# Optimization experiments

Hardware: AMD Instinct MI355X
Metric: run time of the kernel (lower is better)

Reference implementation:

```python
import jax, jax.numpy as jnp
import numpy as np
from jax import lax

V, E, H, K = 100000, 256, 512, 12
B, T = 64, 256
START, END, PAD = 10, 11, 0
NEG = -100000.0


def setup_inputs() -> dict:
    key = jax.random.key(0)
    ks = jax.random.split(key, 16)
    Hd = H // 2
    def n(k, shape, s=0.1):
        return jax.random.normal(k, shape, jnp.float32) * s
    sentence = jax.random.randint(ks[0], (B, T), 0, V)
    sentence_chars = jnp.zeros((B, T, 16), jnp.int32)
    emb = jax.random.normal(ks[1], (V, E), jnp.float32)
    Wih_f, Whh_f = n(ks[2], (4 * Hd, E)), n(ks[3], (4 * Hd, Hd))
    bih_f, bhh_f = n(ks[4], (4 * Hd,)), n(ks[5], (4 * Hd,))
    Wih_b, Whh_b = n(ks[6], (4 * Hd, E)), n(ks[7], (4 * Hd, Hd))
    bih_b, bhh_b = n(ks[8], (4 * Hd,)), n(ks[9], (4 * Hd,))
    Wp, bp = n(ks[10], (K, H)), n(ks[11], (K,))
    # transitions[i, j] = score of transitioning from tag j to tag i
    trans = jax.random.normal(ks[12], (K, K), jnp.float32)
    trans = trans.at[START, :].set(NEG)
    trans = trans.at[:, END].set(NEG)
    trans = trans.at[:, PAD].set(NEG)
    trans = trans.at[PAD, :].set(NEG)
    trans = trans.at[PAD, PAD].set(0.0)
    trans = trans.at[PAD, END].set(0.0)
    h0 = jax.random.normal(ks[13], (2, B, Hd), jnp.float32)
    c0 = jax.random.normal(ks[14], (2, B, Hd), jnp.float32)
    return dict(sentence=sentence, sentence_chars=sentence_chars, emb=emb,
                Wih_f=Wih_f, Whh_f=Whh_f, bih_f=bih_f, bhh_f=bhh_f,
                Wih_b=Wih_b, Whh_b=Whh_b, bih_b=bih_b, bhh_b=bhh_b,
                Wp=Wp, bp=bp, transitions=trans, h0=h0, c0=c0)


def _lstm_dir(x, Wih, Whh, bih, bhh, h, c, reverse):
    # x: [B, T, E] -> hs: [B, T, Hd]; PyTorch LSTM gate order i,f,g,o
    def step(carry, xt):
        h, c = carry
        g = xt @ Wih.T + bih + h @ Whh.T + bhh
        i, f, gg, o = jnp.split(g, 4, axis=-1)
        c = jax.nn.sigmoid(f) * c + jax.nn.sigmoid(i) * jnp.tanh(gg)
        h = jax.nn.sigmoid(o) * jnp.tanh(c)
        return (h, c), h
    _, hs = lax.scan(step, (h, c), jnp.swapaxes(x, 0, 1), reverse=reverse)
    return jnp.swapaxes(hs, 0, 1)


def _viterbi(features, transitions, lengths):
    b, t, k = features.shape
    score0 = jnp.full((b, k), -10000.0, features.dtype).at[:, START].set(0.0)
    def step(score, feat_t):
        m = score[:, None, :] + transitions[None]  # [B, K(to), K(from)]
        bptr = jnp.argmax(m, axis=-1)              # [B, K]
        new = jnp.max(m, axis=-1) + feat_t
        return new, bptr
    final, bptrs = lax.scan(step, score0, jnp.swapaxes(features, 0, 1))  # bptrs [T,B,K]
    best_score = jnp.max(final, axis=-1)
    best_tag = jnp.argmax(final, axis=-1)
    ts = jnp.arange(t)
    def backtrack(x, inp):
        tt, bp = inp  # bp: [B, K]
        emit = x      # p_t (valid where tt < length)
        nxt = jnp.take_along_axis(bp, x[:, None], axis=1)[:, 0]
        x = jnp.where(tt < lengths, nxt, x)
        return x, emit
    _, ps = lax.scan(backtrack, best_tag, (ts, bptrs), reverse=True)  # [T, B]
    paths = jnp.swapaxes(ps, 0, 1)
    paths = jnp.where(jnp.arange(t)[None, :] < lengths[:, None], paths, -1)
    return paths, best_score


def reference(sentence, sentence_chars, emb, Wih_f, Whh_f, bih_f, bhh_f,
              Wih_b, Whh_b, bih_b, bhh_b, Wp, bp, transitions, h0, c0):
    mask = sentence > 0
    lengths = mask.sum(axis=1)
    x = emb[sentence]  # [B, T, E]
    hf = _lstm_dir(x, Wih_f, Whh_f, bih_f, bhh_f, h0[0], c0[0], False)
    hb = _lstm_dir(x, Wih_b, Whh_b, bih_b, bhh_b, h0[1], c0[1], True)
    feats = jnp.concatenate([hf, hb], axis=-1) @ Wp.T + bp  # [B, T, K]
    paths, best_score = _viterbi(feats, transitions, lengths)
    return paths, best_score
```

## Files before the change

### kernel.cpp

```cpp
#include <hip/hip_runtime.h>


#define NB 64
#define NT 256
#define NKTAG 12
#define START_TAG 10
#define KK_SLAB 32
#define KK_REG 16
#define KK_STRM 8

typedef unsigned short u16;
typedef _Float16 half2v __attribute__((ext_vector_type(2)));
typedef _Float16 half8 __attribute__((ext_vector_type(8)));
typedef float f32x4 __attribute__((ext_vector_type(4)));

__device__ __forceinline__ float b2f(u16 u) {
  union { unsigned int i; float f; } v; v.i = ((unsigned int)u) << 16; return v.f;
}
__device__ __forceinline__ u16 f2b(float f) {
  union { float f; unsigned int i; } v; v.f = f;
  unsigned int r = v.i + 0x7FFFu + ((v.i >> 16) & 1u);
  return (u16)(r >> 16);
}
__device__ __forceinline__ u16 f2h(float f) {
  union { _Float16 h; u16 u; } v; v.h = (_Float16)f; return v.u;
}
__device__ __forceinline__ unsigned int pkh(float x, float y) {
  return (unsigned int)f2h(x) | ((unsigned int)f2h(y) << 16);
}
__device__ __forceinline__ float fsig(float x) { return 1.0f / (1.0f + __expf(-x)); }
__device__ __forceinline__ float ftanh(float x) { return 2.0f / (1.0f + __expf(-2.0f * x)) - 1.0f; }

__device__ __forceinline__ float dot2h(unsigned int a, unsigned int b, float c) {
#if __has_builtin(__builtin_amdgcn_fdot2)
  union { unsigned int u; half2v h; } va, vb;
  va.u = a; vb.u = b;
  return __builtin_amdgcn_fdot2(va.h, vb.h, c, false);
#else
  float d;
  asm("v_dot2_f32_f16 %0, %1, %2, %3" : "=v"(d) : "v"(a), "v"(b), "v"(c));
  return d;
#endif
}

__global__ __launch_bounds__(256) void pack_whh(const float* __restrict__ Whf,
                                                const float* __restrict__ Whb,
                                                uint4* __restrict__ WT) {
  int gid = blockIdx.x * 256 + threadIdx.x;
  int d = gid >> 15;
  int rem = gid & 32767;
  int kk = rem >> 8, j = rem & 255;
  const float* W = d ? Whb : Whf;
  int k0 = kk * 2;
  uint4 o;
  o.x = pkh(W[(size_t)j * 256 + k0],         W[(size_t)j * 256 + k0 + 1]);
  o.y = pkh(W[(size_t)(j + 256) * 256 + k0], W[(size_t)(j + 256) * 256 + k0 + 1]);
  o.z = pkh(W[(size_t)(j + 512) * 256 + k0], W[(size_t)(j + 512) * 256 + k0 + 1]);
  o.w = pkh(W[(size_t)(j + 768) * 256 + k0], W[(size_t)(j + 768) * 256 + k0 + 1]);
  WT[gid] = o;
}

__global__ __launch_bounds__(256) void gemm_x(const int* __restrict__ sent,
                                              const float* __restrict__ emb,
                                              const float* __restrict__ Wf,
                                              const float* __restrict__ Wb,
                                              const float* __restrict__ bihf,
                                              const float* __restrict__ bhhf,
                                              const float* __restrict__ bihb,
                                              const float* __restrict__ bhhb,
                                              u16* __restrict__ X4) {
  __shared__ _Float16 A_lds[128][40];
  __shared__ _Float16 B_lds[64][40];
  __shared__ int tok[128];
  int tid = threadIdx.x;
  int in = blockIdx.x;
  int im = blockIdx.y;
  if (tid < 128) tok[tid] = sent[im * 128 + tid];

  int w = tid >> 6, l = tid & 63;
  int lrow = l & 15, lk = l >> 4;
  f32x4 acc[2][4];
#pragma unroll
  for (int mt = 0; mt < 2; ++mt)
#pragma unroll
    for (int nt = 0; nt < 4; ++nt) acc[mt][nt] = (f32x4)0.0f;

  int arow = tid >> 1, akh = tid & 1;
  int brow = tid & 63, bkq = tid >> 6;
  int ngb = in * 64 + brow;
  const float* wrow = (ngb < 1024) ? (Wf + (size_t)ngb * 256) : (Wb + (size_t)(ngb - 1024) * 256);

  for (int kc = 0; kc < 8; ++kc) {
    int k0 = kc * 32;
    __syncthreads();
    {
      const float* ap = emb + (size_t)tok[arow] * 256 + k0 + akh * 16;
#pragma unroll
      for (int q = 0; q < 2; ++q) {
        float4 v0 = *(const float4*)(ap + q * 8);
        float4 v1 = *(const float4*)(ap + q * 8 + 4);
        uint4 pk;
        pk.x = pkh(v0.x, v0.y); pk.y = pkh(v0.z, v0.w);
        pk.z = pkh(v1.x, v1.y); pk.w = pkh(v1.z, v1.w);
        *(uint4*)&A_lds[arow][akh * 16 + q * 8] = pk;
      }
    }
    {
      float4 v0 = *(const float4*)(wrow + k0 + bkq * 8);
      float4 v1 = *(const float4*)(wrow + k0 + bkq * 8 + 4);
      uint4 pk;
      pk.x = pkh(v0.x, v0.y); pk.y = pkh(v0.z, v0.w);
      pk.z = pkh(v1.x, v1.y); pk.w = pkh(v1.z, v1.w);
      *(uint4*)&B_lds[brow][bkq * 8] = pk;
    }
    __syncthreads();
    half8 af[2], bf[4];
#pragma unroll
    for (int mt = 0; mt < 2; ++mt)
      af[mt] = *(const half8*)&A_lds[w * 32 + mt * 16 + lrow][lk * 8];
#pragma unroll
    for (int nt = 0; nt < 4; ++nt)
      bf[nt] = *(const half8*)&B_lds[nt * 16 + lrow][lk * 8];
#pragma unroll
    for (int mt = 0; mt < 2; ++mt)
#pragma unroll
      for (int nt = 0; nt < 4; ++nt)
        acc[mt][nt] = __builtin_amdgcn_mfma_f32_16x16x32_f16(af[mt], bf[nt], acc[mt][nt], 0, 0, 0);
  }
#pragma unroll
  for (int nt = 0; nt < 4; ++nt) {
    int n = in * 64 + nt * 16 + lrow;
    int d = n >> 10, rr = n & 1023;
    int gate = rr >> 8, j = rr & 255;
    float bias = d ? (bihb[rr] + bhhb[rr]) : (bihf[rr] + bhhf[rr]);
#pragma unroll
    for (int mt = 0; mt < 2; ++mt) {
#pragma unroll
      for (int r = 0; r < 4; ++r) {
        int i = im * 128 + w * 32 + mt * 16 + lk * 4 + r;
        int bb = i >> 8, tt = i & 255;
        size_t o = ((((size_t)d * NT + tt) * NB + bb) * 256 + j) * 4 + gate;
        X4[o] = f2b(acc[mt][nt][r] + bias);
      }
    }
  }
}

__global__ __launch_bounds__(1024, 4) void lstm_scan(const uint4* __restrict__ WT,
                                                     const ushort4* __restrict__ X4,
                                                     const float* __restrict__ h0,
                                                     const float* __restrict__ c0,
                                                     void* __restrict__ H, int h32) {
  int d = blockIdx.x >> 6, b = blockIdx.x & 63;
  int tid = threadIdx.x;
  int jj = tid & 255, g = tid >> 8;
  __shared__ uint4 wlds[KK_SLAB * 256];
  __shared__ uint4 h2s4[32];
  __shared__ float4 plds[3][256];
  const uint4* Ws = WT + (size_t)d * 32768;
  for (int e = tid; e < KK_SLAB * 256; e += 1024) wlds[e] = Ws[e];
  uint4 wreg[KK_REG];
#pragma unroll
  for (int r = 0; r < KK_REG; ++r)
    wreg[r] = Ws[(size_t)(KK_SLAB + g * KK_REG + r) * 256 + jj];
  float c = 0.f;
  if (g == 0) c = c0[((size_t)d * NB + b) * 256 + jj];
  if (tid < 256) ((u16*)h2s4)[tid] = f2h(h0[((size_t)d * NB + b) * 256 + tid]);
  __syncthreads();
  for (int s = 0; s < NT; ++s) {
    int t = d ? (NT - 1 - s) : s;
    ushort4 xg = make_ushort4(0, 0, 0, 0);
    if (g == 0) xg = X4[(((size_t)d * NT + t) * NB + b) * 256 + jj];
    float ai = 0.f, af = 0.f, ag = 0.f, ao = 0.f;
    {
      uint4 hc0 = h2s4[24 + g * 2], hc1 = h2s4[24 + g * 2 + 1];
      unsigned int hp[8] = {hc0.x, hc0.y, hc0.z, hc0.w, hc1.x, hc1.y, hc1.z, hc1.w};
      const uint4* Wp_ = Ws + (size_t)(96 + g * 8) * 256 + jj;
#pragma unroll
      for (int u = 0; u < KK_STRM; ++u) {
        uint4 wv = Wp_[(size_t)u * 256];
        ai = dot2h(wv.x, hp[u], ai); af = dot2h(wv.y, hp[u], af);
        ag = dot2h(wv.z, hp[u], ag); ao = dot2h(wv.w, hp[u], ao);
      }
    }
    {
      uint4 ha0 = h2s4[g * 2], ha1 = h2s4[g * 2 + 1];
      unsigned int hp[8] = {ha0.x, ha0.y, ha0.z, ha0.w, ha1.x, ha1.y, ha1.z, ha1.w};
#pragma unroll
      for (int r = 0; r < 8; ++r) {
        uint4 wv = wlds[((g * 8 + r) << 8) | jj];
        ai = dot2h(wv.x, hp[r], ai); af = dot2h(wv.y, hp[r], af);
        ag = dot2h(wv.z, hp[r], ag); ao = dot2h(wv.w, hp[r], ao);
      }
    }
    {
      uint4 hb0 = h2s4[8 + g * 4], hb1 = h2s4[8 + g * 4 + 1];
      uint4 hb2 = h2s4[8 + g * 4 + 2], hb3 = h2s4[8 + g * 4 + 3];
      unsigned int hp[16] = {hb0.x, hb0.y, hb0.z, hb0.w, hb1.x, hb1.y, hb1.z, hb1.w,
                             hb2.x, hb2.y, hb2.z, hb2.w, hb3.x, hb3.y, hb3.z, hb3.w};
#pragma unroll
      for (int r = 0; r < KK_REG; ++r) {
        uint4 wv = wreg[r];
        ai = dot2h(wv.x, hp[r], ai); af = dot2h(wv.y, hp[r], af);
        ag = dot2h(wv.z, hp[r], ag); ao = dot2h(wv.w, hp[r], ao);
      }
    }
    if (g) plds[g - 1][jj] = make_float4(ai, af, ag, ao);
    __syncthreads();
    if (g == 0) {
      float4 p0 = plds[0][jj], p1 = plds[1][jj], p2 = plds[2][jj];
      ai += p0.x + p1.x + p2.x + b2f(xg.x);
      af += p0.y + p1.y + p2.y + b2f(xg.y);
      ag += p0.z + p1.z + p2.z + b2f(xg.z);
      ao += p0.w + p1.w + p2.w + b2f(xg.w);
      float ii = fsig(ai), ff = fsig(af), gg = ftanh(ag), oo = fsig(ao);
      c = ff * c + ii * gg;
      float h = oo * ftanh(c);
      ((u16*)h2s4)[jj] = f2h(h);
      size_t ho = (((size_t)d * NB + b) * NT + t) * 256 + jj;
      if (h32) ((float*)H)[ho] = h; else ((u16*)H)[ho] = f2b(h);
    }
    __syncthreads();
  }
}

__global__ __launch_bounds__(384) void feats_kernel(const void* __restrict__ H, int h32,
                                                    const float* __restrict__ Wp,
                                                    const float* __restrict__ bp,
                                                    float* __restrict__ FT) {
  __shared__ float hbuf[32][516];
  int tid = threadIdx.x;
  int i0 = blockIdx.x * 32;
  for (int idx = tid; idx < 32 * 512; idx += 384) {
    int row = idx >> 9, col = idx & 511;
    int i = i0 + row;
    int b = i >> 8, t = i & 255;
    int dd = col >> 8, jj = col & 255;
    size_t ho = (((size_t)dd * NB + b) * NT + t) * 256 + jj;
    hbuf[row][col] = h32 ? ((const float*)H)[ho] : b2f(((const u16*)H)[ho]);
  }
  __syncthreads();
  int row = tid / 12, k = tid - row * 12;
  const float* wp = Wp + (size_t)k * 512;
  float s = 0.f;
  for (int ccol = 0; ccol < 512; ++ccol) s += hbuf[row][ccol] * wp[ccol];
  int i = i0 + row;
  FT[(size_t)i * NKTAG + k] = s + bp[k];
}

__global__ __launch_bounds__(64) void viterbi_kernel(const float* __restrict__ FT,
                                                     const float* __restrict__ trans,
                                                     const int* __restrict__ sent,
                                                     float* __restrict__ out) {
  int b = blockIdx.x, tid = threadIdx.x;
  __shared__ float trans_s[12][12];
  __shared__ float s_s[12];
  __shared__ unsigned char bp_s[256][12];
  __shared__ int path_s[256];
  for (int idx = tid; idx < 144; idx += 64) trans_s[idx / 12][idx % 12] = trans[idx];
  int cnt = 0;
#pragma unroll
  for (int q = 0; q < 4; ++q) cnt += (sent[b * NT + q * 64 + tid] > 0) ? 1 : 0;
  for (int off = 32; off; off >>= 1) cnt += __shfl_down(cnt, off);
  int len = __shfl(cnt, 0);
  if (tid < 12) s_s[tid] = (tid == START_TAG) ? 0.f : -10000.f;
  __syncthreads();
  for (int t = 0; t < NT; ++t) {
    float best = 0.f, f = 0.f;
    int barg = 0;
    if (tid < 12) {
      f = FT[((size_t)b * NT + t) * NKTAG + tid];
      best = s_s[0] + trans_s[tid][0];
      barg = 0;
#pragma unroll
      for (int fr = 1; fr < 12; ++fr) {
        float v = s_s[fr] + trans_s[tid][fr];
        if (v > best) { best = v; barg = fr; }
      }
    }
    __syncthreads();
    if (tid < 12) {
      s_s[tid] = best + f;
      bp_s[t][tid] = (unsigned char)barg;
    }
    __syncthreads();
  }
  if (tid == 0) {
    float bs = s_s[0];
    int bt = 0;
    for (int k = 1; k < 12; ++k)
      if (s_s[k] > bs) { bs = s_s[k]; bt = k; }
    out[NB * NT + b] = bs;
    int x = bt;
    for (int tt = NT - 1; tt >= 0; --tt) {
      path_s[tt] = x;
      int nxt = bp_s[tt][x];
      if (tt < len) x = nxt;
    }
  }
  __syncthreads();
#pragma unroll
  for (int q = 0; q < 4; ++q) {
    int t = q * 64 + tid;
    out[b * NT + t] = (t < len) ? (float)path_s[t] : -1.0f;
  }
}

extern "C" void kernel_launch(void* const* d_in, const int* in_sizes, int n_in,
                              void* d_out, int out_size, void* d_ws, size_t ws_size,
                              hipStream_t stream) {
  (void)in_sizes; (void)n_in; (void)out_size;
  const int*   sent  = (const int*)d_in[0];
  const float* emb   = (const float*)d_in[2];
  const float* Wih_f = (const float*)d_in[3];
  const float* Whh_f = (const float*)d_in[4];
  const float* bih_f = (const float*)d_in[5];
  const float* bhh_f = (const float*)d_in[6];
  const float* Wih_b = (const float*)d_in[7];
  const float* Whh_b = (const float*)d_in[8];
  const float* bih_b = (const float*)d_in[9];
  const float* bhh_b = (const float*)d_in[10];
  const float* Wp    = (const float*)d_in[11];
  const float* bp    = (const float*)d_in[12];
  const float* trans = (const float*)d_in[13];
  const float* h0    = (const float*)d_in[14];
  const float* c0    = (const float*)d_in[15];
  float* out = (float*)d_out;

  char* w = (char*)d_ws;
  u16*   X4  = (u16*)w;
  uint4* WTH = (uint4*)(w + 67108864);
  float* FT  = (float*)(w + 67108864 + 1048576);
  void*  H   = (void*)(w + 67108864 + 1048576 + 786432);
  const size_t base = 67108864 + 1048576 + 786432;
  int h32 = (ws_size >= base + (size_t)33554432) ? 1 : 0;

  pack_whh<<<dim3(256), dim3(256), 0, stream>>>(Whh_f, Whh_b, WTH);
  gemm_x<<<dim3(32, 128), dim3(256), 0, stream>>>(sent, emb, Wih_f, Wih_b,
                                                  bih_f, bhh_f, bih_b, bhh_b, X4);
  lstm_scan<<<dim3(128), dim3(1024), 0, stream>>>(WTH, (const ushort4*)X4, h0, c0, H, h32);
  feats_kernel<<<dim3(512), dim3(384), 0, stream>>>(H, h32, Wp, bp, FT);
  viterbi_kernel<<<dim3(64), dim3(64), 0, stream>>>(FT, trans, sent, out);
}
```

Measured before the change: 658.8 us.

## Coalesce gemm_x output via LDS staging and use fp16 hidden states in feats

```diff
diff --git a/kernel.cpp b/kernel.cpp
--- a/kernel.cpp
+++ b/kernel.cpp
@@ -45,7 +45,17 @@
 
 __global__ __launch_bounds__(256) void pack_whh(const float* __restrict__ Whf,
                                                 const float* __restrict__ Whb,
-                                                uint4* __restrict__ WT) {
+                                                const float* __restrict__ Wp,
+                                                uint4* __restrict__ WT,
+                                                unsigned int* __restrict__ WpH) {
+  if (blockIdx.x == 256) {
+    for (int it = 0; it < 12; ++it) {
+      int idx = it * 256 + threadIdx.x;
+      int k = idx >> 8, cc = idx & 255;
+      WpH[idx] = pkh(Wp[(size_t)k * 512 + 2 * cc], Wp[(size_t)k * 512 + 2 * cc + 1]);
+    }
+    return;
+  }
   int gid = blockIdx.x * 256 + threadIdx.x;
   int d = gid >> 15;
   int rem = gid & 32767;
@@ -72,9 +82,11 @@
   __shared__ _Float16 A_lds[128][40];
   __shared__ _Float16 B_lds[64][40];
   __shared__ int tok[128];
+  __shared__ u16 Xs[128][80];
   int tid = threadIdx.x;
   int in = blockIdx.x;
   int im = blockIdx.y;
+  int d = in >> 4, j0 = (in & 15) * 16;
   if (tid < 128) tok[tid] = sent[im * 128 + tid];
 
   int w = tid >> 6, l = tid & 63;
@@ -87,8 +99,8 @@
 
   int arow = tid >> 1, akh = tid & 1;
   int brow = tid & 63, bkq = tid >> 6;
-  int ngb = in * 64 + brow;
-  const float* wrow = (ngb < 1024) ? (Wf + (size_t)ngb * 256) : (Wb + (size_t)(ngb - 1024) * 256);
+  int r_w = ((brow >> 4) << 8) + j0 + (brow & 15);
+  const float* wrow = (d ? Wb : Wf) + (size_t)r_w * 256;
 
   for (int kc = 0; kc < 8; ++kc) {
     int k0 = kc * 32;
@@ -127,30 +139,40 @@
       for (int nt = 0; nt < 4; ++nt)
         acc[mt][nt] = __builtin_amdgcn_mfma_f32_16x16x32_f16(af[mt], bf[nt], acc[mt][nt], 0, 0, 0);
   }
+  float bias[4];
 #pragma unroll
   for (int nt = 0; nt < 4; ++nt) {
-    int n = in * 64 + nt * 16 + lrow;
-    int d = n >> 10, rr = n & 1023;
-    int gate = rr >> 8, j = rr & 255;
-    float bias = d ? (bihb[rr] + bhhb[rr]) : (bihf[rr] + bhhf[rr]);
-#pragma unroll
-    for (int mt = 0; mt < 2; ++mt) {
-#pragma unroll
-      for (int r = 0; r < 4; ++r) {
-        int i = im * 128 + w * 32 + mt * 16 + lk * 4 + r;
-        int bb = i >> 8, tt = i & 255;
-        size_t o = ((((size_t)d * NT + tt) * NB + bb) * 256 + j) * 4 + gate;
-        X4[o] = f2b(acc[mt][nt][r] + bias);
-      }
-    }
-  }
+    int rr = nt * 256 + j0 + lrow;
+    bias[nt] = d ? (bihb[rr] + bhhb[rr]) : (bihf[rr] + bhhf[rr]);
+  }
+  __syncthreads();
+#pragma unroll
+  for (int mt = 0; mt < 2; ++mt)
+#pragma unroll
+    for (int r = 0; r < 4; ++r) {
+      int row = w * 32 + mt * 16 + lk * 4 + r;
+      uint2 pk;
+      pk.x = (unsigned int)f2b(acc[mt][0][r] + bias[0]) |
+             ((unsigned int)f2b(acc[mt][1][r] + bias[1]) << 16);
+      pk.y = (unsigned int)f2b(acc[mt][2][r] + bias[2]) |
+             ((unsigned int)f2b(acc[mt][3][r] + bias[3]) << 16);
+      *(uint2*)&Xs[row][lrow * 4] = pk;
+    }
+  __syncthreads();
+  int frow = tid >> 1, fh = tid & 1;
+  int i = im * 128 + frow;
+  int bb = i >> 8, tt = i & 255;
+  size_t base = (((size_t)d * NT + tt) * NB + bb) * 1024 + (size_t)j0 * 4 + fh * 32;
+#pragma unroll
+  for (int q = 0; q < 4; ++q)
+    *(uint4*)&X4[base + q * 8] = *(const uint4*)&Xs[frow][fh * 32 + q * 8];
 }
 
 __global__ __launch_bounds__(1024, 4) void lstm_scan(const uint4* __restrict__ WT,
                                                      const ushort4* __restrict__ X4,
                                                      const float* __restrict__ h0,
                                                      const float* __restrict__ c0,
-                                                     void* __restrict__ H, int h32) {
+                                                     u16* __restrict__ H) {
   int d = blockIdx.x >> 6, b = blockIdx.x & 63;
   int tid = threadIdx.x;
   int jj = tid & 255, g = tid >> 8;
@@ -216,34 +238,44 @@
       float ii = fsig(ai), ff = fsig(af), gg = ftanh(ag), oo = fsig(ao);
       c = ff * c + ii * gg;
       float h = oo * ftanh(c);
-      ((u16*)h2s4)[jj] = f2h(h);
-      size_t ho = (((size_t)d * NB + b) * NT + t) * 256 + jj;
-      if (h32) ((float*)H)[ho] = h; else ((u16*)H)[ho] = f2b(h);
-    }
-    __syncthreads();
-  }
-}
-
-__global__ __launch_bounds__(384) void feats_kernel(const void* __restrict__ H, int h32,
-                                                    const float* __restrict__ Wp,
+      u16 hu = f2h(h);
+      ((u16*)h2s4)[jj] = hu;
+      H[(((size_t)d * NB + b) * NT + t) * 256 + jj] = hu;
+    }
+    __syncthreads();
+  }
+}
+
+__global__ __launch_bounds__(384) void feats_kernel(const u16* __restrict__ H,
+                                                    const unsigned int* __restrict__ WpH,
                                                     const float* __restrict__ bp,
                                                     float* __restrict__ FT) {
-  __shared__ float hbuf[32][516];
+  __shared__ uint4 hbuf[32][65];
+  __shared__ uint4 wbuf[64][12];
   int tid = threadIdx.x;
   int i0 = blockIdx.x * 32;
-  for (int idx = tid; idx < 32 * 512; idx += 384) {
-    int row = idx >> 9, col = idx & 511;
+  for (int idx = tid; idx < 768; idx += 384) {
+    int it = idx / 12, k = idx - it * 12;
+    wbuf[it][k] = ((const uint4*)WpH)[k * 64 + it];
+  }
+  for (int idx = tid; idx < 2048; idx += 384) {
+    int row = idx >> 6, c4 = idx & 63;
     int i = i0 + row;
     int b = i >> 8, t = i & 255;
-    int dd = col >> 8, jj = col & 255;
-    size_t ho = (((size_t)dd * NB + b) * NT + t) * 256 + jj;
-    hbuf[row][col] = h32 ? ((const float*)H)[ho] : b2f(((const u16*)H)[ho]);
+    int dd = c4 >> 5, cc = c4 & 31;
+    const uint4* hp = (const uint4*)(H + (((size_t)dd * NB + b) * NT + t) * 256);
+    hbuf[row][c4] = hp[cc];
   }
   __syncthreads();
   int row = tid / 12, k = tid - row * 12;
-  const float* wp = Wp + (size_t)k * 512;
   float s = 0.f;
-  for (int ccol = 0; ccol < 512; ++ccol) s += hbuf[row][ccol] * wp[ccol];
+#pragma unroll 8
+  for (int it = 0; it < 64; ++it) {
+    uint4 h4 = hbuf[row][it];
+    uint4 w4 = wbuf[it][k];
+    s = dot2h(h4.x, w4.x, s); s = dot2h(h4.y, w4.y, s);
+    s = dot2h(h4.z, w4.z, s); s = dot2h(h4.w, w4.w, s);
+  }
   int i = i0 + row;
   FT[(size_t)i * NKTAG + k] = s + bp[k];
 }
@@ -309,7 +341,7 @@
 extern "C" void kernel_launch(void* const* d_in, const int* in_sizes, int n_in,
                               void* d_out, int out_size, void* d_ws, size_t ws_size,
                               hipStream_t stream) {
-  (void)in_sizes; (void)n_in; (void)out_size;
+  (void)in_sizes; (void)n_in; (void)out_size; (void)ws_size;
   const int*   sent  = (const int*)d_in[0];
   const float* emb   = (const float*)d_in[2];
   const float* Wih_f = (const float*)d_in[3];
@@ -331,14 +363,13 @@
   u16*   X4  = (u16*)w;
   uint4* WTH = (uint4*)(w + 67108864);
   float* FT  = (float*)(w + 67108864 + 1048576);
-  void*  H   = (void*)(w + 67108864 + 1048576 + 786432);
-  const size_t base = 67108864 + 1048576 + 786432;
-  int h32 = (ws_size >= base + (size_t)33554432) ? 1 : 0;
-
-  pack_whh<<<dim3(256), dim3(256), 0, stream>>>(Whh_f, Whh_b, WTH);
+  unsigned int* WpH = (unsigned int*)(w + 68943872);
+  u16*   H   = (u16*)(w + 68956160);
+
+  pack_whh<<<dim3(257), dim3(256), 0, stream>>>(Whh_f, Whh_b, Wp, WTH, WpH);
   gemm_x<<<dim3(32, 128), dim3(256), 0, stream>>>(sent, emb, Wih_f, Wih_b,
                                                   bih_f, bhh_f, bih_b, bhh_b, X4);
-  lstm_scan<<<dim3(128), dim3(1024), 0, stream>>>(WTH, (const ushort4*)X4, h0, c0, H, h32);
-  feats_kernel<<<dim3(512), dim3(384), 0, stream>>>(H, h32, Wp, bp, FT);
+  lstm_scan<<<dim3(128), dim3(1024), 0, stream>>>(WTH, (const ushort4*)X4, h0, c0, H);
+  feats_kernel<<<dim3(512), dim3(384), 0, stream>>>(H, WpH, bp, FT);
   viterbi_kernel<<<dim3(64), dim3(64), 0, stream>>>(FT, trans, sent, out);
 }
```

New measurement: 599.4 us. -9.0%, faster.
